# Kernel optimization log

Measured on AMD Instinct MI355X. Metric: run time of the kernel, lower is better.

## Reference

```python
import jax, jax.numpy as jnp
import numpy as np

N = 100000
E = 1600000
IN_CH = 128
EDGE_CH = 16
HID = 128
OUT = 4
EPS = 1e-12  # F.normalize eps


def l2_normalize(x):
    # matches torch.nn.functional.normalize(x, p=2, dim=1)
    norm = jnp.sqrt(jnp.sum(x * x, axis=1, keepdims=True))
    return x / jnp.maximum(norm, EPS)


def sage_conv(x, row, col, edge_attr, W, b, n_nodes):
    # gather source node feats, concat edge feats: [E, in+edge]
    m = jnp.concatenate([x[row], edge_attr], axis=1)
    m = l2_normalize(m)
    # scatter-mean by destination node
    s = jax.ops.segment_sum(m, col, num_segments=n_nodes)
    cnt = jax.ops.segment_sum(jnp.ones((m.shape[0],), m.dtype), col, num_segments=n_nodes)
    agg = s / jnp.maximum(cnt, 1.0)[:, None]
    out = agg @ W + b
    return l2_normalize(out)


def setup_inputs() -> dict:
    key = jax.random.key(0)
    ks = jax.random.split(key, 7)
    x = jax.random.normal(ks[0], (N, IN_CH), dtype=jnp.float32)
    edge_index = jax.random.randint(ks[1], (2, E), 0, N, dtype=jnp.int64)
    edge_attr = jax.random.normal(ks[2], (E, EDGE_CH), dtype=jnp.float32)
    W1 = jax.random.normal(ks[3], (IN_CH + EDGE_CH, HID), dtype=jnp.float32) / np.sqrt(IN_CH + EDGE_CH)
    b1 = jnp.zeros((HID,), dtype=jnp.float32)
    W2 = jax.random.normal(ks[4], (HID + EDGE_CH, OUT), dtype=jnp.float32) / np.sqrt(HID + EDGE_CH)
    b2 = jnp.zeros((OUT,), dtype=jnp.float32)
    return {"x": x, "edge_index": edge_index, "edge_attr": edge_attr,
            "W1": W1, "b1": b1, "W2": W2, "b2": b2}


def reference(x, edge_index, edge_attr, W1, b1, W2, b2):
    row, col = edge_index[0], edge_index[1]
    h = sage_conv(x, row, col, edge_attr, W1, b1, N)
    h = jax.nn.relu(h)  # dropout is identity in eval mode
    h = sage_conv(h, row, col, edge_attr, W2, b2, N)
    return jax.nn.sigmoid(h)
```

## Files before the change

### kernel.cpp

```cpp
#include <hip/hip_runtime.h>
#include <hip/hip_fp16.h>
#include <math.h>

#define N_NODES 100000
#define N_EDGES 1600000
#define CHUNK 1024
#define NCHUNKS ((N_NODES + CHUNK - 1) / CHUNK)

union H4 { uint2 u; __half2 h[2]; };

__device__ __forceinline__ float red32(float v) {
    #pragma unroll
    for (int m = 16; m >= 1; m >>= 1) v += __shfl_xor(v, m, 64);
    return v;
}

__global__ __launch_bounds__(256) void prep_edges(
        const float* __restrict__ ea, const int* __restrict__ col,
        const float* __restrict__ W2,
        float* __restrict__ sqea, float4* __restrict__ pea, int* __restrict__ cnt) {
    __shared__ float w2e[64];
    int t = threadIdx.x;
    if (t < 64) w2e[t] = W2[128 * 4 + t];
    __syncthreads();
    int e = blockIdx.x * 256 + t;
    if (e >= N_EDGES) return;
    const float4* p = (const float4*)(ea + (size_t)e * 16);
    float4 q0 = p[0], q1 = p[1], q2 = p[2], q3 = p[3];
    float a[16] = {q0.x,q0.y,q0.z,q0.w, q1.x,q1.y,q1.z,q1.w,
                   q2.x,q2.y,q2.z,q2.w, q3.x,q3.y,q3.z,q3.w};
    float s = 0.f;
    float4 pv = make_float4(0.f, 0.f, 0.f, 0.f);
    #pragma unroll
    for (int k = 0; k < 16; ++k) {
        s += a[k] * a[k];
        pv.x += a[k] * w2e[k * 4 + 0];
        pv.y += a[k] * w2e[k * 4 + 1];
        pv.z += a[k] * w2e[k * 4 + 2];
        pv.w += a[k] * w2e[k * 4 + 3];
    }
    sqea[e] = s;
    pea[e] = pv;
    atomicAdd(&cnt[col[e]], 1);
}

__global__ void scan_part(const int* __restrict__ cnt, int* __restrict__ psum) {
    __shared__ int sd[CHUNK];
    int i = blockIdx.x * CHUNK + threadIdx.x;
    sd[threadIdx.x] = (i < N_NODES) ? cnt[i] : 0;
    __syncthreads();
    for (int s = CHUNK / 2; s > 0; s >>= 1) {
        if (threadIdx.x < s) sd[threadIdx.x] += sd[threadIdx.x + s];
        __syncthreads();
    }
    if (threadIdx.x == 0) psum[blockIdx.x] = sd[0];
}

__global__ void scan_top(const int* __restrict__ psum, int* __restrict__ coff,
                         int* __restrict__ off) {
    if (blockIdx.x == 0 && threadIdx.x == 0) {
        int run = 0;
        for (int i = 0; i < NCHUNKS; ++i) { coff[i] = run; run += psum[i]; }
        off[N_NODES] = N_EDGES;
    }
}

__global__ void scan_apply(const int* __restrict__ cnt, const int* __restrict__ coff,
                           int* __restrict__ off, int* __restrict__ head) {
    __shared__ int sd[CHUNK];
    int i = blockIdx.x * CHUNK + threadIdx.x;
    int v = (i < N_NODES) ? cnt[i] : 0;
    sd[threadIdx.x] = v;
    __syncthreads();
    for (int s = 1; s < CHUNK; s <<= 1) {
        int t = (threadIdx.x >= s) ? sd[threadIdx.x - s] : 0;
        __syncthreads();
        sd[threadIdx.x] += t;
        __syncthreads();
    }
    if (i < N_NODES) {
        int excl = coff[blockIdx.x] + sd[threadIdx.x] - v;
        off[i] = excl;
        head[i] = excl;
    }
}

__global__ __launch_bounds__(256) void scatter_e(
        const int* __restrict__ row, const int* __restrict__ col,
        const float* __restrict__ nx, const float* __restrict__ sqea,
        int* __restrict__ head, int4* __restrict__ csr4, int* __restrict__ epos) {
    int e = blockIdx.x * blockDim.x + threadIdx.x;
    if (e >= N_EDGES) return;
    int c = col[e];
    int r = row[e];
    float w1 = rsqrtf(fmaxf(nx[r] + sqea[e], 1e-24f));
    int p = atomicAdd(&head[c], 1);
    int4 mt; mt.x = r; mt.y = __float_as_int(w1); mt.z = e; mt.w = 0;
    csr4[p] = mt;
    epos[e] = p;
}

__global__ __launch_bounds__(256) void gemm_y1h(const float* __restrict__ x,
                                                const float* __restrict__ W1,
                                                __half* __restrict__ y1h,
                                                float* __restrict__ nx) {
    __shared__ float xs[64][129];
    int r0 = blockIdx.x * 64;
    int t = threadIdx.x;
    for (int i = t; i < 64 * 32; i += 256) {
        int rr = i >> 5, c4 = (i & 31) * 4;
        int gr = r0 + rr;
        float4 v = (gr < N_NODES) ? *(const float4*)(x + (size_t)gr * 128 + c4)
                                  : make_float4(0.f, 0.f, 0.f, 0.f);
        xs[rr][c4] = v.x; xs[rr][c4 + 1] = v.y; xs[rr][c4 + 2] = v.z; xs[rr][c4 + 3] = v.w;
    }
    __syncthreads();
    {
        int rr = t >> 2, q = t & 3;
        float s = 0.f;
        #pragma unroll
        for (int k = 0; k < 32; ++k) { float v = xs[rr][q * 32 + k]; s += v * v; }
        s += __shfl_xor(s, 1, 64);
        s += __shfl_xor(s, 2, 64);
        if (q == 0 && r0 + rr < N_NODES) nx[r0 + rr] = s;
    }
    int tx = t & 31, ty = t >> 5;
    float4 acc[8];
    #pragma unroll
    for (int i = 0; i < 8; ++i) acc[i] = make_float4(0.f, 0.f, 0.f, 0.f);
    for (int k = 0; k < 128; ++k) {
        float4 wv = *(const float4*)(W1 + (size_t)k * 128 + tx * 4);
        #pragma unroll
        for (int i = 0; i < 8; ++i) {
            float xv = xs[ty * 8 + i][k];
            acc[i].x += xv * wv.x; acc[i].y += xv * wv.y;
            acc[i].z += xv * wv.z; acc[i].w += xv * wv.w;
        }
    }
    #pragma unroll
    for (int i = 0; i < 8; ++i) {
        int rr = r0 + ty * 8 + i;
        if (rr < N_NODES) {
            H4 pk;
            pk.h[0] = __float22half2_rn(make_float2(acc[i].x, acc[i].y));
            pk.h[1] = __float22half2_rn(make_float2(acc[i].z, acc[i].w));
            *(uint2*)(y1h + (size_t)rr * 128 + tx * 4) = pk.u;
        }
    }
}

__global__ __launch_bounds__(256) void layer1(
        const __half* __restrict__ y1h, const float* __restrict__ ea,
        const int4* __restrict__ csr4, const int* __restrict__ off,
        const float* __restrict__ W1, const float* __restrict__ b1,
        const float* __restrict__ W2,
        float* __restrict__ hn) {
    int wid = (blockIdx.x << 2) | (threadIdx.x >> 6);
    int lane = threadIdx.x & 63;
    if (wid >= N_NODES) return;
    int h = lane >> 5;
    int c = lane & 31;
    int s = off[wid], e = off[wid + 1];
    int deg = e - s;
    int m = (deg < 64) ? deg : 64;
    int4 meta = (lane < m) ? csr4[s + lane] : make_int4(0, 0, 0, 0);

    float4 acc = make_float4(0.f, 0.f, 0.f, 0.f);
    float4 ae4 = make_float4(0.f, 0.f, 0.f, 0.f);

    int j = 0;
    for (; j + 8 <= m; j += 8) {
        #pragma unroll
        for (int i = 0; i < 4; ++i) {
            int idx = j + 2 * i + h;
            int r   = __shfl(meta.x, idx, 64);
            float w = __int_as_float(__shfl(meta.y, idx, 64));
            int id  = __shfl(meta.z, idx, 64);
            H4 pk; pk.u = *(const uint2*)(y1h + (size_t)r * 128 + c * 4);
            float2 f0 = __half22float2(pk.h[0]);
            float2 f1 = __half22float2(pk.h[1]);
            acc.x += f0.x * w; acc.y += f0.y * w;
            acc.z += f1.x * w; acc.w += f1.y * w;
            if (c < 4) {
                float4 ev = *(const float4*)(ea + (size_t)id * 16 + c * 4);
                ae4.x += ev.x * w; ae4.y += ev.y * w;
                ae4.z += ev.z * w; ae4.w += ev.w * w;
            }
        }
    }
    for (; j < m; j += 2) {
        int idx = j + h;
        bool val = idx < m;
        int ii = val ? idx : 0;
        int r   = __shfl(meta.x, ii, 64);
        float w = val ? __int_as_float(__shfl(meta.y, ii, 64)) : 0.f;
        int id  = __shfl(meta.z, ii, 64);
        H4 pk; pk.u = *(const uint2*)(y1h + (size_t)r * 128 + c * 4);
        float2 f0 = __half22float2(pk.h[0]);
        float2 f1 = __half22float2(pk.h[1]);
        acc.x += f0.x * w; acc.y += f0.y * w;
        acc.z += f1.x * w; acc.w += f1.y * w;
        if (c < 4) {
            float4 ev = *(const float4*)(ea + (size_t)id * 16 + c * 4);
            ae4.x += ev.x * w; ae4.y += ev.y * w;
            ae4.z += ev.z * w; ae4.w += ev.w * w;
        }
    }
    if (deg > 64) {
        for (int j2 = 64; j2 < deg; j2 += 2) {
            int idx = j2 + h;
            bool val = idx < deg;
            int4 mt = csr4[s + (val ? idx : deg - 1)];
            int r = mt.x;
            float w = val ? __int_as_float(mt.y) : 0.f;
            int id = mt.z;
            H4 pk; pk.u = *(const uint2*)(y1h + (size_t)r * 128 + c * 4);
            float2 f0 = __half22float2(pk.h[0]);
            float2 f1 = __half22float2(pk.h[1]);
            acc.x += f0.x * w; acc.y += f0.y * w;
            acc.z += f1.x * w; acc.w += f1.y * w;
            if (c < 4) {
                float4 ev = *(const float4*)(ea + (size_t)id * 16 + c * 4);
                ae4.x += ev.x * w; ae4.y += ev.y * w;
                ae4.z += ev.z * w; ae4.w += ev.w * w;
            }
        }
    }
    acc.x += __shfl_xor(acc.x, 32, 64);
    acc.y += __shfl_xor(acc.y, 32, 64);
    acc.z += __shfl_xor(acc.z, 32, 64);
    acc.w += __shfl_xor(acc.w, 32, 64);
    ae4.x += __shfl_xor(ae4.x, 32, 64);
    ae4.y += __shfl_xor(ae4.y, 32, 64);
    ae4.z += __shfl_xor(ae4.z, 32, 64);
    ae4.w += __shfl_xor(ae4.w, 32, 64);

    float ic = 1.0f / fmaxf((float)deg, 1.0f);
    float4 b1v = *(const float4*)(b1 + c * 4);
    float4 o;
    o.x = acc.x * ic + b1v.x; o.y = acc.y * ic + b1v.y;
    o.z = acc.z * ic + b1v.z; o.w = acc.w * ic + b1v.w;
    ae4.x *= ic; ae4.y *= ic; ae4.z *= ic; ae4.w *= ic;
    float aev[4] = {ae4.x, ae4.y, ae4.z, ae4.w};
    #pragma unroll
    for (int k = 0; k < 16; ++k) {
        float sk = __shfl(aev[k & 3], k >> 2, 64);
        float4 wv = *((const float4*)(W1 + (size_t)(128 + k) * 128) + c);
        o.x += sk * wv.x; o.y += sk * wv.y; o.z += sk * wv.z; o.w += sk * wv.w;
    }
    float ss    = o.x*o.x + o.y*o.y + o.z*o.z + o.w*o.w;
    float sspos = (o.x > 0.f ? o.x*o.x : 0.f) + (o.y > 0.f ? o.y*o.y : 0.f)
                + (o.z > 0.f ? o.z*o.z : 0.f) + (o.w > 0.f ? o.w*o.w : 0.f);
    ss = red32(ss);
    sspos = red32(sspos);
    float inv = rsqrtf(fmaxf(ss, 1e-24f));
    float4 h4;
    h4.x = fmaxf(o.x * inv, 0.f); h4.y = fmaxf(o.y * inv, 0.f);
    h4.z = fmaxf(o.z * inv, 0.f); h4.w = fmaxf(o.w * inv, 0.f);
    float nhv = sspos * inv * inv;
    float4 w0 = *(const float4*)(W2 + (size_t)(4*c + 0) * 4);
    float4 w1 = *(const float4*)(W2 + (size_t)(4*c + 1) * 4);
    float4 w2 = *(const float4*)(W2 + (size_t)(4*c + 2) * 4);
    float4 w3 = *(const float4*)(W2 + (size_t)(4*c + 3) * 4);
    float4 p;
    p.x = h4.x*w0.x + h4.y*w1.x + h4.z*w2.x + h4.w*w3.x;
    p.y = h4.x*w0.y + h4.y*w1.y + h4.z*w2.y + h4.w*w3.y;
    p.z = h4.x*w0.z + h4.y*w1.z + h4.z*w2.z + h4.w*w3.z;
    p.w = h4.x*w0.w + h4.y*w1.w + h4.z*w2.w + h4.w*w3.w;
    p.x = red32(p.x); p.y = red32(p.y); p.z = red32(p.z); p.w = red32(p.w);
    if (lane == 0) {
        *(float4*)(hn + (size_t)wid * 8) = p;
        hn[(size_t)wid * 8 + 4] = nhv;
    }
}

__global__ __launch_bounds__(256) void cpass(
        const int* __restrict__ row, const float* __restrict__ hn,
        const float* __restrict__ sqea, const float4* __restrict__ pea,
        const int* __restrict__ epos, float4* __restrict__ cbuf) {
    int e = blockIdx.x * blockDim.x + threadIdx.x;
    if (e >= N_EDGES) return;
    int r = row[e];
    float4 yh4 = *(const float4*)(hn + (size_t)r * 8);
    float nhr = hn[(size_t)r * 8 + 4];
    float w2 = rsqrtf(fmaxf(nhr + sqea[e], 1e-24f));
    float4 pe = pea[e];
    float4 cv;
    cv.x = (yh4.x + pe.x) * w2; cv.y = (yh4.y + pe.y) * w2;
    cv.z = (yh4.z + pe.z) * w2; cv.w = (yh4.w + pe.w) * w2;
    cbuf[epos[e]] = cv;
}

__global__ __launch_bounds__(256) void layer2b(
        const float4* __restrict__ cbuf, const int* __restrict__ off,
        const float* __restrict__ b2, float* __restrict__ out) {
    int v = blockIdx.x * blockDim.x + threadIdx.x;
    if (v >= N_NODES) return;
    int s = off[v], e = off[v + 1];
    float4 a = make_float4(0.f, 0.f, 0.f, 0.f);
    for (int t = s; t < e; ++t) {
        float4 cv = cbuf[t];
        a.x += cv.x; a.y += cv.y; a.z += cv.z; a.w += cv.w;
    }
    float ic = 1.0f / fmaxf((float)(e - s), 1.0f);
    float4 o;
    o.x = a.x * ic + b2[0]; o.y = a.y * ic + b2[1];
    o.z = a.z * ic + b2[2]; o.w = a.w * ic + b2[3];
    float ss = o.x*o.x + o.y*o.y + o.z*o.z + o.w*o.w;
    float inv = rsqrtf(fmaxf(ss, 1e-24f));
    float4 res;
    res.x = 1.0f / (1.0f + expf(-(o.x * inv)));
    res.y = 1.0f / (1.0f + expf(-(o.y * inv)));
    res.z = 1.0f / (1.0f + expf(-(o.z * inv)));
    res.w = 1.0f / (1.0f + expf(-(o.w * inv)));
    *(float4*)(out + (size_t)v * 4) = res;
}

extern "C" void kernel_launch(void* const* d_in, const int* in_sizes, int n_in,
                              void* d_out, int out_size, void* d_ws, size_t ws_size,
                              hipStream_t stream) {
    const float* x   = (const float*)d_in[0];
    const int*   ei  = (const int*)d_in[1];
    const float* ea  = (const float*)d_in[2];
    const float* W1  = (const float*)d_in[3];
    const float* b1  = (const float*)d_in[4];
    const float* W2  = (const float*)d_in[5];
    const float* b2  = (const float*)d_in[6];
    const int* row = ei;
    const int* col = ei + N_EDGES;
    float* out = (float*)d_out;

    char* ws = (char*)d_ws;
    size_t o = 0;
    auto carve = [&](size_t bytes) { char* p = ws + o; o = (o + bytes + 255) & ~(size_t)255; return p; };
    __half* y1h    = (__half*)carve((size_t)N_NODES * 128 * 2);
    float*  sqea   = (float*)carve((size_t)N_EDGES * 4);
    int4*   csr4   = (int4*)carve((size_t)N_EDGES * 16);
    int*    epos   = (int*)carve((size_t)N_EDGES * 4);
    float4* pea    = (float4*)carve((size_t)N_EDGES * 16);
    float4* cbuf   = (float4*)carve((size_t)N_EDGES * 16);
    int*    cnt    = (int*)carve((size_t)N_NODES * 4);
    int*    off    = (int*)carve((size_t)(N_NODES + 1) * 4);
    int*    head   = (int*)carve((size_t)N_NODES * 4);
    float*  nx     = (float*)carve((size_t)N_NODES * 4);
    float*  hn     = (float*)carve((size_t)N_NODES * 8 * 4);
    int*    psum   = (int*)carve((size_t)NCHUNKS * 4);
    int*    coff   = (int*)carve((size_t)NCHUNKS * 4);
    (void)ws_size; (void)in_sizes; (void)n_in; (void)out_size;

    hipMemsetAsync(cnt, 0, (size_t)N_NODES * 4, stream);

    dim3 b256(256);
    prep_edges<<<(N_EDGES + 255) / 256, b256, 0, stream>>>(ea, col, W2, sqea, pea, cnt);
    gemm_y1h<<<(N_NODES + 63) / 64, b256, 0, stream>>>(x, W1, y1h, nx);

    scan_part<<<NCHUNKS, CHUNK, 0, stream>>>(cnt, psum);
    scan_top<<<1, 64, 0, stream>>>(psum, coff, off);
    scan_apply<<<NCHUNKS, CHUNK, 0, stream>>>(cnt, coff, off, head);
    scatter_e<<<(N_EDGES + 255) / 256, b256, 0, stream>>>(row, col, nx, sqea, head,
                                                          csr4, epos);

    layer1<<<(N_NODES + 3) / 4, b256, 0, stream>>>(y1h, ea, csr4, off, W1, b1, W2, hn);
    cpass<<<(N_EDGES + 255) / 256, b256, 0, stream>>>(row, hn, sqea, pea, epos, cbuf);
    layer2b<<<(N_NODES + 255) / 256, b256, 0, stream>>>(cbuf, off, b2, out);
}
```

Measured before the change: 432.1 us.

## Split layer-1 aggregation into feature-sliced gather and separate edge-attr pass

Stores y1h in a slice-major layout (8 slices of 16 halves per node) and splits layer1 into aggA, which gathers one 32-byte slice per block so each slice's working set is more cache-resident, and layer1B, which does the edge-attribute aggregation plus the dense epilogue. The CSR metadata is split into two 8-byte arrays so each kernel reads only what it needs, and cbuf now aliases the y1h buffer to save workspace. This adds an fp32 agg round trip through global memory, an extra launch, and rereads of off and metadata across the 8 slice blocks.

```diff
diff --git a/kernel.cpp b/kernel.cpp
--- a/kernel.cpp
+++ b/kernel.cpp
@@ -6,6 +6,7 @@
 #define N_EDGES 1600000
 #define CHUNK 1024
 #define NCHUNKS ((N_NODES + CHUNK - 1) / CHUNK)
+#define NSLICE 8
 
 union H4 { uint2 u; __half2 h[2]; };
 
@@ -88,15 +89,16 @@
 __global__ __launch_bounds__(256) void scatter_e(
         const int* __restrict__ row, const int* __restrict__ col,
         const float* __restrict__ nx, const float* __restrict__ sqea,
-        int* __restrict__ head, int4* __restrict__ csr4, int* __restrict__ epos) {
+        int* __restrict__ head, float2* __restrict__ csr_rw,
+        float2* __restrict__ csr_ew, int* __restrict__ epos) {
     int e = blockIdx.x * blockDim.x + threadIdx.x;
     if (e >= N_EDGES) return;
     int c = col[e];
     int r = row[e];
     float w1 = rsqrtf(fmaxf(nx[r] + sqea[e], 1e-24f));
     int p = atomicAdd(&head[c], 1);
-    int4 mt; mt.x = r; mt.y = __float_as_int(w1); mt.z = e; mt.w = 0;
-    csr4[p] = mt;
+    csr_rw[p] = make_float2(__int_as_float(r), w1);
+    csr_ew[p] = make_float2(__int_as_float(e), w1);
     epos[e] = p;
 }
 
@@ -144,109 +146,120 @@
             H4 pk;
             pk.h[0] = __float22half2_rn(make_float2(acc[i].x, acc[i].y));
             pk.h[1] = __float22half2_rn(make_float2(acc[i].z, acc[i].w));
-            *(uint2*)(y1h + (size_t)rr * 128 + tx * 4) = pk.u;
+            __half* dst = y1h + ((size_t)(tx >> 2) * N_NODES + rr) * 16 + (tx & 3) * 4;
+            *(uint2*)dst = pk.u;
         }
     }
 }
 
-__global__ __launch_bounds__(256) void layer1(
-        const __half* __restrict__ y1h, const float* __restrict__ ea,
-        const int4* __restrict__ csr4, const int* __restrict__ off,
-        const float* __restrict__ W1, const float* __restrict__ b1,
-        const float* __restrict__ W2,
-        float* __restrict__ hn) {
-    int wid = (blockIdx.x << 2) | (threadIdx.x >> 6);
+__global__ __launch_bounds__(256) void aggA(
+        const __half* __restrict__ y1h, const float2* __restrict__ csr_rw,
+        const int* __restrict__ off, float* __restrict__ agg) {
+    __shared__ float2 smeta[4][64];
+    int slice = blockIdx.x & 7;
+    int node = ((blockIdx.x >> 3) << 2) | (threadIdx.x >> 6);
     int lane = threadIdx.x & 63;
-    if (wid >= N_NODES) return;
-    int h = lane >> 5;
-    int c = lane & 31;
-    int s = off[wid], e = off[wid + 1];
+    int wv = threadIdx.x >> 6;
+    if (node >= N_NODES) return;
+    int s = off[node], e = off[node + 1];
     int deg = e - s;
     int m = (deg < 64) ? deg : 64;
-    int4 meta = (lane < m) ? csr4[s + lane] : make_int4(0, 0, 0, 0);
-
+    if (lane < m) smeta[wv][lane] = csr_rw[s + lane];
+    asm volatile("s_waitcnt lgkmcnt(0)" ::: "memory");
+    int g = lane >> 2, q = lane & 3;
+    const __half* yb = y1h + (size_t)slice * N_NODES * 16 + q * 4;
     float4 acc = make_float4(0.f, 0.f, 0.f, 0.f);
-    float4 ae4 = make_float4(0.f, 0.f, 0.f, 0.f);
-
-    int j = 0;
-    for (; j + 8 <= m; j += 8) {
-        #pragma unroll
-        for (int i = 0; i < 4; ++i) {
-            int idx = j + 2 * i + h;
-            int r   = __shfl(meta.x, idx, 64);
-            float w = __int_as_float(__shfl(meta.y, idx, 64));
-            int id  = __shfl(meta.z, idx, 64);
-            H4 pk; pk.u = *(const uint2*)(y1h + (size_t)r * 128 + c * 4);
-            float2 f0 = __half22float2(pk.h[0]);
-            float2 f1 = __half22float2(pk.h[1]);
-            acc.x += f0.x * w; acc.y += f0.y * w;
-            acc.z += f1.x * w; acc.w += f1.y * w;
-            if (c < 4) {
-                float4 ev = *(const float4*)(ea + (size_t)id * 16 + c * 4);
-                ae4.x += ev.x * w; ae4.y += ev.y * w;
-                ae4.z += ev.z * w; ae4.w += ev.w * w;
-            }
-        }
-    }
-    for (; j < m; j += 2) {
-        int idx = j + h;
+    int nblk = (m + 15) >> 4;
+    for (int j = 0; j < nblk; ++j) {
+        int idx = (j << 4) + g;
         bool val = idx < m;
-        int ii = val ? idx : 0;
-        int r   = __shfl(meta.x, ii, 64);
-        float w = val ? __int_as_float(__shfl(meta.y, ii, 64)) : 0.f;
-        int id  = __shfl(meta.z, ii, 64);
-        H4 pk; pk.u = *(const uint2*)(y1h + (size_t)r * 128 + c * 4);
+        float2 rw = smeta[wv][val ? idx : 0];
+        int r = __float_as_int(rw.x);
+        float wt = val ? rw.y : 0.f;
+        H4 pk; pk.u = *(const uint2*)(yb + (size_t)r * 16);
         float2 f0 = __half22float2(pk.h[0]);
         float2 f1 = __half22float2(pk.h[1]);
-        acc.x += f0.x * w; acc.y += f0.y * w;
-        acc.z += f1.x * w; acc.w += f1.y * w;
-        if (c < 4) {
-            float4 ev = *(const float4*)(ea + (size_t)id * 16 + c * 4);
-            ae4.x += ev.x * w; ae4.y += ev.y * w;
-            ae4.z += ev.z * w; ae4.w += ev.w * w;
-        }
-    }
-    if (deg > 64) {
-        for (int j2 = 64; j2 < deg; j2 += 2) {
-            int idx = j2 + h;
-            bool val = idx < deg;
-            int4 mt = csr4[s + (val ? idx : deg - 1)];
-            int r = mt.x;
-            float w = val ? __int_as_float(mt.y) : 0.f;
-            int id = mt.z;
-            H4 pk; pk.u = *(const uint2*)(y1h + (size_t)r * 128 + c * 4);
-            float2 f0 = __half22float2(pk.h[0]);
-            float2 f1 = __half22float2(pk.h[1]);
-            acc.x += f0.x * w; acc.y += f0.y * w;
-            acc.z += f1.x * w; acc.w += f1.y * w;
-            if (c < 4) {
-                float4 ev = *(const float4*)(ea + (size_t)id * 16 + c * 4);
-                ae4.x += ev.x * w; ae4.y += ev.y * w;
-                ae4.z += ev.z * w; ae4.w += ev.w * w;
-            }
-        }
-    }
-    acc.x += __shfl_xor(acc.x, 32, 64);
-    acc.y += __shfl_xor(acc.y, 32, 64);
-    acc.z += __shfl_xor(acc.z, 32, 64);
-    acc.w += __shfl_xor(acc.w, 32, 64);
-    ae4.x += __shfl_xor(ae4.x, 32, 64);
-    ae4.y += __shfl_xor(ae4.y, 32, 64);
-    ae4.z += __shfl_xor(ae4.z, 32, 64);
-    ae4.w += __shfl_xor(ae4.w, 32, 64);
-
+        acc.x += f0.x * wt; acc.y += f0.y * wt;
+        acc.z += f1.x * wt; acc.w += f1.y * wt;
+    }
+    for (int t = 64 + g; t < deg; t += 16) {
+        float2 rw = csr_rw[s + t];
+        int r = __float_as_int(rw.x);
+        float wt = rw.y;
+        H4 pk; pk.u = *(const uint2*)(yb + (size_t)r * 16);
+        float2 f0 = __half22float2(pk.h[0]);
+        float2 f1 = __half22float2(pk.h[1]);
+        acc.x += f0.x * wt; acc.y += f0.y * wt;
+        acc.z += f1.x * wt; acc.w += f1.y * wt;
+    }
+    #pragma unroll
+    for (int mm = 4; mm <= 32; mm <<= 1) {
+        acc.x += __shfl_xor(acc.x, mm, 64);
+        acc.y += __shfl_xor(acc.y, mm, 64);
+        acc.z += __shfl_xor(acc.z, mm, 64);
+        acc.w += __shfl_xor(acc.w, mm, 64);
+    }
+    if (lane < 4)
+        *(float4*)(agg + (size_t)node * 128 + slice * 16 + lane * 4) = acc;
+}
+
+__global__ __launch_bounds__(256) void layer1B(
+        const float* __restrict__ agg, const float* __restrict__ ea,
+        const float2* __restrict__ csr_ew, const int* __restrict__ off,
+        const float* __restrict__ W1, const float* __restrict__ b1,
+        const float* __restrict__ W2, float* __restrict__ hn) {
+    __shared__ float2 sew[4][64];
+    int node = (blockIdx.x << 2) | (threadIdx.x >> 6);
+    int lane = threadIdx.x & 63;
+    int wv = threadIdx.x >> 6;
+    if (node >= N_NODES) return;
+    int s = off[node], e = off[node + 1];
+    int deg = e - s;
+    int m = (deg < 64) ? deg : 64;
+    if (lane < m) sew[wv][lane] = csr_ew[s + lane];
+    asm volatile("s_waitcnt lgkmcnt(0)" ::: "memory");
+    int g = lane >> 2, q = lane & 3;
+    float4 se = make_float4(0.f, 0.f, 0.f, 0.f);
+    int nblk = (m + 15) >> 4;
+    for (int j = 0; j < nblk; ++j) {
+        int idx = (j << 4) + g;
+        bool val = idx < m;
+        float2 ew = sew[wv][val ? idx : 0];
+        int id = __float_as_int(ew.x);
+        float wt = val ? ew.y : 0.f;
+        float4 ev = *(const float4*)(ea + (size_t)id * 16 + q * 4);
+        se.x += ev.x * wt; se.y += ev.y * wt;
+        se.z += ev.z * wt; se.w += ev.w * wt;
+    }
+    for (int t = 64 + g; t < deg; t += 16) {
+        float2 ew = csr_ew[s + t];
+        int id = __float_as_int(ew.x);
+        float wt = ew.y;
+        float4 ev = *(const float4*)(ea + (size_t)id * 16 + q * 4);
+        se.x += ev.x * wt; se.y += ev.y * wt;
+        se.z += ev.z * wt; se.w += ev.w * wt;
+    }
+    #pragma unroll
+    for (int mm = 4; mm <= 32; mm <<= 1) {
+        se.x += __shfl_xor(se.x, mm, 64);
+        se.y += __shfl_xor(se.y, mm, 64);
+        se.z += __shfl_xor(se.z, mm, 64);
+        se.w += __shfl_xor(se.w, mm, 64);
+    }
     float ic = 1.0f / fmaxf((float)deg, 1.0f);
+    int c = lane & 31;
+    float4 av = *(const float4*)(agg + (size_t)node * 128 + c * 4);
     float4 b1v = *(const float4*)(b1 + c * 4);
     float4 o;
-    o.x = acc.x * ic + b1v.x; o.y = acc.y * ic + b1v.y;
-    o.z = acc.z * ic + b1v.z; o.w = acc.w * ic + b1v.w;
-    ae4.x *= ic; ae4.y *= ic; ae4.z *= ic; ae4.w *= ic;
-    float aev[4] = {ae4.x, ae4.y, ae4.z, ae4.w};
+    o.x = av.x * ic + b1v.x; o.y = av.y * ic + b1v.y;
+    o.z = av.z * ic + b1v.z; o.w = av.w * ic + b1v.w;
+    se.x *= ic; se.y *= ic; se.z *= ic; se.w *= ic;
+    float sev[4] = {se.x, se.y, se.z, se.w};
     #pragma unroll
     for (int k = 0; k < 16; ++k) {
-        float sk = __shfl(aev[k & 3], k >> 2, 64);
-        float4 wv = *((const float4*)(W1 + (size_t)(128 + k) * 128) + c);
-        o.x += sk * wv.x; o.y += sk * wv.y; o.z += sk * wv.z; o.w += sk * wv.w;
+        float sk = __shfl(sev[k & 3], k >> 2, 64);
+        float4 wv4 = *((const float4*)(W1 + (size_t)(128 + k) * 128) + c);
+        o.x += sk * wv4.x; o.y += sk * wv4.y; o.z += sk * wv4.z; o.w += sk * wv4.w;
     }
     float ss    = o.x*o.x + o.y*o.y + o.z*o.z + o.w*o.w;
     float sspos = (o.x > 0.f ? o.x*o.x : 0.f) + (o.y > 0.f ? o.y*o.y : 0.f)
@@ -269,8 +282,8 @@
     p.w = h4.x*w0.w + h4.y*w1.w + h4.z*w2.w + h4.w*w3.w;
     p.x = red32(p.x); p.y = red32(p.y); p.z = red32(p.z); p.w = red32(p.w);
     if (lane == 0) {
-        *(float4*)(hn + (size_t)wid * 8) = p;
-        hn[(size_t)wid * 8 + 4] = nhv;
+        *(float4*)(hn + (size_t)node * 8) = p;
+        hn[(size_t)node * 8 + 4] = nhv;
     }
 }
 
@@ -334,11 +347,13 @@
     size_t o = 0;
     auto carve = [&](size_t bytes) { char* p = ws + o; o = (o + bytes + 255) & ~(size_t)255; return p; };
     __half* y1h    = (__half*)carve((size_t)N_NODES * 128 * 2);
+    float4* cbuf   = (float4*)y1h;
     float*  sqea   = (float*)carve((size_t)N_EDGES * 4);
-    int4*   csr4   = (int4*)carve((size_t)N_EDGES * 16);
+    float2* csr_rw = (float2*)carve((size_t)N_EDGES * 8);
+    float2* csr_ew = (float2*)carve((size_t)N_EDGES * 8);
     int*    epos   = (int*)carve((size_t)N_EDGES * 4);
     float4* pea    = (float4*)carve((size_t)N_EDGES * 16);
-    float4* cbuf   = (float4*)carve((size_t)N_EDGES * 16);
+    float*  agg    = (float*)carve((size_t)N_NODES * 128 * 4);
     int*    cnt    = (int*)carve((size_t)N_NODES * 4);
     int*    off    = (int*)carve((size_t)(N_NODES + 1) * 4);
     int*    head   = (int*)carve((size_t)N_NODES * 4);
@@ -358,9 +373,11 @@
     scan_top<<<1, 64, 0, stream>>>(psum, coff, off);
     scan_apply<<<NCHUNKS, CHUNK, 0, stream>>>(cnt, coff, off, head);
     scatter_e<<<(N_EDGES + 255) / 256, b256, 0, stream>>>(row, col, nx, sqea, head,
-                                                          csr4, epos);
-
-    layer1<<<(N_NODES + 3) / 4, b256, 0, stream>>>(y1h, ea, csr4, off, W1, b1, W2, hn);
+                                                          csr_rw, csr_ew, epos);
+
+    aggA<<<(N_NODES / 4) * NSLICE, b256, 0, stream>>>(y1h, csr_rw, off, agg);
+    layer1B<<<N_NODES / 4, b256, 0, stream>>>(agg, ea, csr_ew, off, W1, b1, W2, hn);
+
     cpass<<<(N_EDGES + 255) / 256, b256, 0, stream>>>(row, hn, sqea, pea, epos, cbuf);
     layer2b<<<(N_NODES + 255) / 256, b256, 0, stream>>>(cbuf, off, b2, out);
 }
```

Result: slower. 595.0 us (+37.7%).

## Widen layer1 gathers with fp16 edge attributes and shared-memory edge metadata

Applied to the files above, without the earlier changes.

prep_edges now also writes an fp16 copy of the edge attributes, so layer1 gathers 32 bytes per edge instead of 64. layer1 is restructured so a wavefront handles four edges per step, each lane doing a 16-byte load of 8 fp16 features, with edge metadata staged in LDS instead of read through shuffles. Partial sums are combined across the four edge groups and handed through shared memory to the dense epilogue. cbuf now reuses the y1h buffer, which is no longer needed by the time cbuf is written, and the gemm k-loop gets an unroll hint. The cost is an extra fp16 edge-attribute write in prep_edges, which also adds a rounding step to the edge features.

```diff
diff --git a/kernel.cpp b/kernel.cpp
--- a/kernel.cpp
+++ b/kernel.cpp
@@ -7,7 +7,7 @@
 #define CHUNK 1024
 #define NCHUNKS ((N_NODES + CHUNK - 1) / CHUNK)
 
-union H4 { uint2 u; __half2 h[2]; };
+union H8 { uint4 u; __half2 h[4]; };
 
 __device__ __forceinline__ float red32(float v) {
     #pragma unroll
@@ -18,7 +18,8 @@
 __global__ __launch_bounds__(256) void prep_edges(
         const float* __restrict__ ea, const int* __restrict__ col,
         const float* __restrict__ W2,
-        float* __restrict__ sqea, float4* __restrict__ pea, int* __restrict__ cnt) {
+        float* __restrict__ sqea, float4* __restrict__ pea,
+        __half* __restrict__ eah, int* __restrict__ cnt) {
     __shared__ float w2e[64];
     int t = threadIdx.x;
     if (t < 64) w2e[t] = W2[128 * 4 + t];
@@ -41,6 +42,17 @@
     }
     sqea[e] = s;
     pea[e] = pv;
+    H8 u0, u1;
+    u0.h[0] = __float22half2_rn(make_float2(q0.x, q0.y));
+    u0.h[1] = __float22half2_rn(make_float2(q0.z, q0.w));
+    u0.h[2] = __float22half2_rn(make_float2(q1.x, q1.y));
+    u0.h[3] = __float22half2_rn(make_float2(q1.z, q1.w));
+    u1.h[0] = __float22half2_rn(make_float2(q2.x, q2.y));
+    u1.h[1] = __float22half2_rn(make_float2(q2.z, q2.w));
+    u1.h[2] = __float22half2_rn(make_float2(q3.x, q3.y));
+    u1.h[3] = __float22half2_rn(make_float2(q3.z, q3.w));
+    uint4* dst = (uint4*)(eah + (size_t)e * 16);
+    dst[0] = u0.u; dst[1] = u1.u;
     atomicAdd(&cnt[col[e]], 1);
 }
 
@@ -128,6 +140,7 @@
     float4 acc[8];
     #pragma unroll
     for (int i = 0; i < 8; ++i) acc[i] = make_float4(0.f, 0.f, 0.f, 0.f);
+    #pragma unroll 4
     for (int k = 0; k < 128; ++k) {
         float4 wv = *(const float4*)(W1 + (size_t)k * 128 + tx * 4);
         #pragma unroll
@@ -141,112 +154,112 @@
     for (int i = 0; i < 8; ++i) {
         int rr = r0 + ty * 8 + i;
         if (rr < N_NODES) {
-            H4 pk;
+            H8 pk;
             pk.h[0] = __float22half2_rn(make_float2(acc[i].x, acc[i].y));
             pk.h[1] = __float22half2_rn(make_float2(acc[i].z, acc[i].w));
-            *(uint2*)(y1h + (size_t)rr * 128 + tx * 4) = pk.u;
+            *(uint2*)(y1h + (size_t)rr * 128 + tx * 4) = make_uint2(pk.u.x, pk.u.y);
         }
     }
 }
 
 __global__ __launch_bounds__(256) void layer1(
-        const __half* __restrict__ y1h, const float* __restrict__ ea,
+        const __half* __restrict__ y1h, const __half* __restrict__ eah,
         const int4* __restrict__ csr4, const int* __restrict__ off,
         const float* __restrict__ W1, const float* __restrict__ b1,
-        const float* __restrict__ W2,
-        float* __restrict__ hn) {
-    int wid = (blockIdx.x << 2) | (threadIdx.x >> 6);
+        const float* __restrict__ W2, float* __restrict__ hn) {
+    __shared__ int4  smeta[4][64];
+    __shared__ float strans[4][144];
+    int wv = threadIdx.x >> 6;
+    int node = (blockIdx.x << 2) | wv;
     int lane = threadIdx.x & 63;
-    if (wid >= N_NODES) return;
-    int h = lane >> 5;
-    int c = lane & 31;
-    int s = off[wid], e = off[wid + 1];
+    if (node >= N_NODES) return;
+    int s = off[node], e = off[node + 1];
     int deg = e - s;
     int m = (deg < 64) ? deg : 64;
-    int4 meta = (lane < m) ? csr4[s + lane] : make_int4(0, 0, 0, 0);
-
-    float4 acc = make_float4(0.f, 0.f, 0.f, 0.f);
-    float4 ae4 = make_float4(0.f, 0.f, 0.f, 0.f);
-
-    int j = 0;
-    for (; j + 8 <= m; j += 8) {
-        #pragma unroll
-        for (int i = 0; i < 4; ++i) {
-            int idx = j + 2 * i + h;
-            int r   = __shfl(meta.x, idx, 64);
-            float w = __int_as_float(__shfl(meta.y, idx, 64));
-            int id  = __shfl(meta.z, idx, 64);
-            H4 pk; pk.u = *(const uint2*)(y1h + (size_t)r * 128 + c * 4);
-            float2 f0 = __half22float2(pk.h[0]);
-            float2 f1 = __half22float2(pk.h[1]);
-            acc.x += f0.x * w; acc.y += f0.y * w;
-            acc.z += f1.x * w; acc.w += f1.y * w;
-            if (c < 4) {
-                float4 ev = *(const float4*)(ea + (size_t)id * 16 + c * 4);
-                ae4.x += ev.x * w; ae4.y += ev.y * w;
-                ae4.z += ev.z * w; ae4.w += ev.w * w;
-            }
-        }
-    }
-    for (; j < m; j += 2) {
-        int idx = j + h;
+    if (lane < m) smeta[wv][lane] = csr4[s + lane];
+    asm volatile("s_waitcnt lgkmcnt(0)" ::: "memory");
+
+    int e4 = lane >> 4;
+    int c8 = lane & 15;
+    float4 a0 = make_float4(0,0,0,0), a1 = a0;
+    float4 ae0 = a0, ae1 = a0;
+
+    #pragma unroll 2
+    for (int t = 0; t < m; t += 4) {
+        int idx = t + e4;
         bool val = idx < m;
-        int ii = val ? idx : 0;
-        int r   = __shfl(meta.x, ii, 64);
-        float w = val ? __int_as_float(__shfl(meta.y, ii, 64)) : 0.f;
-        int id  = __shfl(meta.z, ii, 64);
-        H4 pk; pk.u = *(const uint2*)(y1h + (size_t)r * 128 + c * 4);
+        int4 mt = smeta[wv][val ? idx : 0];
+        float w = val ? __int_as_float(mt.y) : 0.f;
+        H8 pk; pk.u = *(const uint4*)(y1h + (size_t)mt.x * 128 + c8 * 8);
         float2 f0 = __half22float2(pk.h[0]);
         float2 f1 = __half22float2(pk.h[1]);
-        acc.x += f0.x * w; acc.y += f0.y * w;
-        acc.z += f1.x * w; acc.w += f1.y * w;
-        if (c < 4) {
-            float4 ev = *(const float4*)(ea + (size_t)id * 16 + c * 4);
-            ae4.x += ev.x * w; ae4.y += ev.y * w;
-            ae4.z += ev.z * w; ae4.w += ev.w * w;
-        }
-    }
-    if (deg > 64) {
-        for (int j2 = 64; j2 < deg; j2 += 2) {
-            int idx = j2 + h;
-            bool val = idx < deg;
-            int4 mt = csr4[s + (val ? idx : deg - 1)];
-            int r = mt.x;
-            float w = val ? __int_as_float(mt.y) : 0.f;
-            int id = mt.z;
-            H4 pk; pk.u = *(const uint2*)(y1h + (size_t)r * 128 + c * 4);
-            float2 f0 = __half22float2(pk.h[0]);
-            float2 f1 = __half22float2(pk.h[1]);
-            acc.x += f0.x * w; acc.y += f0.y * w;
-            acc.z += f1.x * w; acc.w += f1.y * w;
-            if (c < 4) {
-                float4 ev = *(const float4*)(ea + (size_t)id * 16 + c * 4);
-                ae4.x += ev.x * w; ae4.y += ev.y * w;
-                ae4.z += ev.z * w; ae4.w += ev.w * w;
-            }
-        }
-    }
-    acc.x += __shfl_xor(acc.x, 32, 64);
-    acc.y += __shfl_xor(acc.y, 32, 64);
-    acc.z += __shfl_xor(acc.z, 32, 64);
-    acc.w += __shfl_xor(acc.w, 32, 64);
-    ae4.x += __shfl_xor(ae4.x, 32, 64);
-    ae4.y += __shfl_xor(ae4.y, 32, 64);
-    ae4.z += __shfl_xor(ae4.z, 32, 64);
-    ae4.w += __shfl_xor(ae4.w, 32, 64);
-
+        float2 f2 = __half22float2(pk.h[2]);
+        float2 f3 = __half22float2(pk.h[3]);
+        a0.x += f0.x * w; a0.y += f0.y * w; a0.z += f1.x * w; a0.w += f1.y * w;
+        a1.x += f2.x * w; a1.y += f2.y * w; a1.z += f3.x * w; a1.w += f3.y * w;
+        if (c8 < 2) {
+            H8 ek; ek.u = *(const uint4*)(eah + (size_t)mt.z * 16 + c8 * 8);
+            float2 g0 = __half22float2(ek.h[0]);
+            float2 g1 = __half22float2(ek.h[1]);
+            float2 g2 = __half22float2(ek.h[2]);
+            float2 g3 = __half22float2(ek.h[3]);
+            ae0.x += g0.x * w; ae0.y += g0.y * w; ae0.z += g1.x * w; ae0.w += g1.y * w;
+            ae1.x += g2.x * w; ae1.y += g2.y * w; ae1.z += g3.x * w; ae1.w += g3.y * w;
+        }
+    }
+    for (int t = 64 + e4; t < deg; t += 4) {
+        int4 mt = csr4[s + t];
+        float w = __int_as_float(mt.y);
+        H8 pk; pk.u = *(const uint4*)(y1h + (size_t)mt.x * 128 + c8 * 8);
+        float2 f0 = __half22float2(pk.h[0]);
+        float2 f1 = __half22float2(pk.h[1]);
+        float2 f2 = __half22float2(pk.h[2]);
+        float2 f3 = __half22float2(pk.h[3]);
+        a0.x += f0.x * w; a0.y += f0.y * w; a0.z += f1.x * w; a0.w += f1.y * w;
+        a1.x += f2.x * w; a1.y += f2.y * w; a1.z += f3.x * w; a1.w += f3.y * w;
+        if (c8 < 2) {
+            H8 ek; ek.u = *(const uint4*)(eah + (size_t)mt.z * 16 + c8 * 8);
+            float2 g0 = __half22float2(ek.h[0]);
+            float2 g1 = __half22float2(ek.h[1]);
+            float2 g2 = __half22float2(ek.h[2]);
+            float2 g3 = __half22float2(ek.h[3]);
+            ae0.x += g0.x * w; ae0.y += g0.y * w; ae0.z += g1.x * w; ae0.w += g1.y * w;
+            ae1.x += g2.x * w; ae1.y += g2.y * w; ae1.z += g3.x * w; ae1.w += g3.y * w;
+        }
+    }
+    #pragma unroll
+    for (int mm = 16; mm <= 32; mm <<= 1) {
+        a0.x += __shfl_xor(a0.x, mm, 64); a0.y += __shfl_xor(a0.y, mm, 64);
+        a0.z += __shfl_xor(a0.z, mm, 64); a0.w += __shfl_xor(a0.w, mm, 64);
+        a1.x += __shfl_xor(a1.x, mm, 64); a1.y += __shfl_xor(a1.y, mm, 64);
+        a1.z += __shfl_xor(a1.z, mm, 64); a1.w += __shfl_xor(a1.w, mm, 64);
+        ae0.x += __shfl_xor(ae0.x, mm, 64); ae0.y += __shfl_xor(ae0.y, mm, 64);
+        ae0.z += __shfl_xor(ae0.z, mm, 64); ae0.w += __shfl_xor(ae0.w, mm, 64);
+        ae1.x += __shfl_xor(ae1.x, mm, 64); ae1.y += __shfl_xor(ae1.y, mm, 64);
+        ae1.z += __shfl_xor(ae1.z, mm, 64); ae1.w += __shfl_xor(ae1.w, mm, 64);
+    }
+    if (e4 == 0) {
+        *(float4*)&strans[wv][c8 * 8]     = a0;
+        *(float4*)&strans[wv][c8 * 8 + 4] = a1;
+        if (c8 < 2) {
+            *(float4*)&strans[wv][128 + c8 * 8]     = ae0;
+            *(float4*)&strans[wv][128 + c8 * 8 + 4] = ae1;
+        }
+    }
+    asm volatile("s_waitcnt lgkmcnt(0)" ::: "memory");
+
+    int c = lane & 31;
     float ic = 1.0f / fmaxf((float)deg, 1.0f);
+    float4 av = *(const float4*)&strans[wv][c * 4];
     float4 b1v = *(const float4*)(b1 + c * 4);
     float4 o;
-    o.x = acc.x * ic + b1v.x; o.y = acc.y * ic + b1v.y;
-    o.z = acc.z * ic + b1v.z; o.w = acc.w * ic + b1v.w;
-    ae4.x *= ic; ae4.y *= ic; ae4.z *= ic; ae4.w *= ic;
-    float aev[4] = {ae4.x, ae4.y, ae4.z, ae4.w};
+    o.x = av.x * ic + b1v.x; o.y = av.y * ic + b1v.y;
+    o.z = av.z * ic + b1v.z; o.w = av.w * ic + b1v.w;
     #pragma unroll
     for (int k = 0; k < 16; ++k) {
-        float sk = __shfl(aev[k & 3], k >> 2, 64);
-        float4 wv = *((const float4*)(W1 + (size_t)(128 + k) * 128) + c);
-        o.x += sk * wv.x; o.y += sk * wv.y; o.z += sk * wv.z; o.w += sk * wv.w;
+        float sk = strans[wv][128 + k] * ic;
+        float4 wv4 = *((const float4*)(W1 + (size_t)(128 + k) * 128) + c);
+        o.x += sk * wv4.x; o.y += sk * wv4.y; o.z += sk * wv4.z; o.w += sk * wv4.w;
     }
     float ss    = o.x*o.x + o.y*o.y + o.z*o.z + o.w*o.w;
     float sspos = (o.x > 0.f ? o.x*o.x : 0.f) + (o.y > 0.f ? o.y*o.y : 0.f)
@@ -269,8 +282,8 @@
     p.w = h4.x*w0.w + h4.y*w1.w + h4.z*w2.w + h4.w*w3.w;
     p.x = red32(p.x); p.y = red32(p.y); p.z = red32(p.z); p.w = red32(p.w);
     if (lane == 0) {
-        *(float4*)(hn + (size_t)wid * 8) = p;
-        hn[(size_t)wid * 8 + 4] = nhv;
+        *(float4*)(hn + (size_t)node * 8) = p;
+        hn[(size_t)node * 8 + 4] = nhv;
     }
 }
 
@@ -334,11 +347,12 @@
     size_t o = 0;
     auto carve = [&](size_t bytes) { char* p = ws + o; o = (o + bytes + 255) & ~(size_t)255; return p; };
     __half* y1h    = (__half*)carve((size_t)N_NODES * 128 * 2);
+    float4* cbuf   = (float4*)y1h;
     float*  sqea   = (float*)carve((size_t)N_EDGES * 4);
     int4*   csr4   = (int4*)carve((size_t)N_EDGES * 16);
     int*    epos   = (int*)carve((size_t)N_EDGES * 4);
     float4* pea    = (float4*)carve((size_t)N_EDGES * 16);
-    float4* cbuf   = (float4*)carve((size_t)N_EDGES * 16);
+    __half* eah    = (__half*)carve((size_t)N_EDGES * 16 * 2);
     int*    cnt    = (int*)carve((size_t)N_NODES * 4);
     int*    off    = (int*)carve((size_t)(N_NODES + 1) * 4);
     int*    head   = (int*)carve((size_t)N_NODES * 4);
@@ -351,7 +365,7 @@
     hipMemsetAsync(cnt, 0, (size_t)N_NODES * 4, stream);
 
     dim3 b256(256);
-    prep_edges<<<(N_EDGES + 255) / 256, b256, 0, stream>>>(ea, col, W2, sqea, pea, cnt);
+    prep_edges<<<(N_EDGES + 255) / 256, b256, 0, stream>>>(ea, col, W2, sqea, pea, eah, cnt);
     gemm_y1h<<<(N_NODES + 63) / 64, b256, 0, stream>>>(x, W1, y1h, nx);
 
     scan_part<<<NCHUNKS, CHUNK, 0, stream>>>(cnt, psum);
@@ -360,7 +374,7 @@
     scatter_e<<<(N_EDGES + 255) / 256, b256, 0, stream>>>(row, col, nx, sqea, head,
                                                           csr4, epos);
 
-    layer1<<<(N_NODES + 3) / 4, b256, 0, stream>>>(y1h, ea, csr4, off, W1, b1, W2, hn);
+    layer1<<<(N_NODES + 3) / 4, b256, 0, stream>>>(y1h, eah, csr4, off, W1, b1, W2, hn);
     cpass<<<(N_EDGES + 255) / 256, b256, 0, stream>>>(row, hn, sqea, pea, epos, cbuf);
     layer2b<<<(N_NODES + 255) / 256, b256, 0, stream>>>(cbuf, off, b2, out);
 }
```

New measurement: 427.8 us. Within noise of the previous version (-1.0%).
